# Performance work log

Hardware: AMD Instinct MI355X
Metric: run time of the kernel (lower is better)

The kernel has to match this reference:

```python
import jax, jax.numpy as jnp
import numpy as np

B, N, D, LAT, EC = 1024, 256, 64, 128, 32


def setup_inputs() -> dict:
    key = jax.random.key(0)
    ks = jax.random.split(key, 8)
    s = lambda d: 1.0 / np.sqrt(d)
    return {
        "local_data": jax.random.normal(ks[0], (B, D), jnp.float32),
        "neighbor_data": jax.random.normal(ks[1], (B, N, D), jnp.float32),
        "Wc": jax.random.normal(ks[2], (D, EC), jnp.float32) * s(D),
        "bc": jnp.zeros((EC,), jnp.float32),
        "Wf": jax.random.normal(ks[3], (D, LAT), jnp.float32) * s(D),
        "bf": jnp.zeros((LAT,), jnp.float32),
        "Wa": jax.random.normal(ks[4], (3 * EC, LAT), jnp.float32) * s(3 * EC),
        "ba": jnp.zeros((LAT,), jnp.float32),
        "Wl": jax.random.normal(ks[5], (LAT, LAT), jnp.float32) * s(LAT),
        "bl": jnp.zeros((LAT,), jnp.float32),
    }


def reference(local_data, neighbor_data, Wc, bc, Wf, bf, Wa, ba, Wl, bl):
    # per-neighbor feature encoder: [B,N,LAT]
    enc_feature = jax.nn.relu(jnp.einsum("bnd,dk->bnk", neighbor_data, Wf) + bf)
    # per-neighbor communication encoder: [B,N,EC]
    enc_comm = jax.nn.relu(jnp.einsum("bnd,dk->bnk", neighbor_data, Wc) + bc)
    # self communication embedding: [B,EC]
    enc_comm_self = jax.nn.relu(local_data @ Wc + bc)
    # broadcast self and neighbor-mean to [B,N,EC]
    self_rep = jnp.broadcast_to(enc_comm_self[:, None, :], enc_comm.shape)
    mean_rep = jnp.broadcast_to(enc_comm.mean(axis=1, keepdims=True), enc_comm.shape)
    cat = jnp.concatenate([self_rep, enc_comm, mean_rep], axis=-1)  # [B,N,3*EC]
    # attention: linear then softmax over neighbor axis (dim=-2)
    att = jax.nn.softmax(jnp.einsum("bnc,ck->bnk", cat, Wa) + ba, axis=1)  # [B,N,LAT]
    # attention-weighted sum over neighbors: [B,LAT]
    aggregated = jnp.einsum("bnk,bnk->bk", att, enc_feature)
    # later layer
    return jax.nn.relu(aggregated @ Wl + bl)
```

## Files before the change

### kernel.cpp

```cpp
#include <hip/hip_runtime.h>

#define NB    256
#define DIN   64
#define LATD  128
#define ECD   32

typedef __attribute__((ext_vector_type(8))) __bf16 bf16x8;
typedef __attribute__((ext_vector_type(2))) __bf16 bf16x2;
typedef __attribute__((ext_vector_type(4))) float f32x4;

#define XS_STRIDE 72
#define EC_STRIDE 40
#define WA_STRIDE 40

#define WS_WC  0
#define WS_WF  (32 * 72)
#define WS_WA  (32 * 72 + 128 * 72)
#define WS_WLT_BYTES 33280

#define LOG2E 1.44269504f

#define MFMA(a, b, c) __builtin_amdgcn_mfma_f32_16x16x32_bf16((a), (b), (c), 0, 0, 0)

__device__ __forceinline__ unsigned short f2bf(float f) {
    unsigned u = __builtin_bit_cast(unsigned, f);
    u += 0x7fffu + ((u >> 16) & 1u);
    return (unsigned short)(u >> 16);
}

__device__ __forceinline__ bf16x2 cvt2(float a, float b) {
#if defined(__has_builtin) && __has_builtin(__builtin_amdgcn_cvt_pk_bf16_f32)
    return __builtin_amdgcn_cvt_pk_bf16_f32(a, b);
#else
    union { unsigned short u[2]; bf16x2 v; } r;
    r.u[0] = f2bf(a); r.u[1] = f2bf(b);
    return r.v;
#endif
}

__device__ __forceinline__ bf16x8 pack8(float4 a, float4 b) {
    union { bf16x2 h[4]; bf16x8 v; } r;
    r.h[0] = cvt2(a.x, a.y); r.h[1] = cvt2(a.z, a.w);
    r.h[2] = cvt2(b.x, b.y); r.h[3] = cvt2(b.z, b.w);
    return r.v;
}

__global__ __launch_bounds__(256) void prep_kernel(
    const float* __restrict__ Wc, const float* __restrict__ Wf,
    const float* __restrict__ Wa, const float* __restrict__ Wl,
    unsigned short* __restrict__ ws)
{
    int t = blockIdx.x * blockDim.x + threadIdx.x;
    int stride = gridDim.x * blockDim.x;
    for (int i = t; i < 32 * 64; i += stride) {
        int n = i >> 6, k = i & 63;
        ws[WS_WC + n * XS_STRIDE + k] = f2bf(Wc[k * ECD + n]);
    }
    for (int i = t; i < 128 * 64; i += stride) {
        int n = i >> 6, k = i & 63;
        ws[WS_WF + n * XS_STRIDE + k] = f2bf(Wf[k * LATD + n]);
    }
    for (int i = t; i < 128 * 32; i += stride) {
        int n = i >> 5, k = i & 31;
        ws[WS_WA + n * WA_STRIDE + k] = f2bf(Wa[(ECD + k) * LATD + n] * LOG2E);
    }
    float* wlt = reinterpret_cast<float*>(reinterpret_cast<char*>(ws) + WS_WLT_BYTES);
    for (int i = t; i < 128 * 128; i += stride) {
        int c = i >> 7, k = i & 127;
        wlt[c * 128 + k] = Wl[k * LATD + c];
    }
}

__global__ __launch_bounds__(512, 8) void arm_main(
    const float* __restrict__ xg,
    const float* __restrict__ bcv,
    const float* __restrict__ bfv,
    const float* __restrict__ blv,
    const unsigned short* __restrict__ ws,
    float* __restrict__ out)
{
    __shared__ unsigned short ecs[NB * EC_STRIDE];
    __shared__ float aggnum[8][LATD];
    __shared__ float aggden[8][LATD];
    __shared__ float aggfull[LATD];
    __shared__ float wlpart[4][LATD];

    const int b    = blockIdx.x;
    const int tid  = threadIdx.x;
    const int lane = tid & 63;
    const int w    = tid >> 6;
    const int l15  = lane & 15;
    const int q    = lane >> 4;

    const float* xb = xg + (size_t)b * NB * DIN;
    bf16x8 xfrag[2][2];
    #pragma unroll
    for (int t = 0; t < 2; ++t) {
        const float* p = xb + (w * 32 + t * 16 + l15) * DIN + q * 8;
        float4 a0 = *reinterpret_cast<const float4*>(p);
        float4 a1 = *reinterpret_cast<const float4*>(p + 4);
        float4 a2 = *reinterpret_cast<const float4*>(p + 32);
        float4 a3 = *reinterpret_cast<const float4*>(p + 36);
        xfrag[t][0] = pack8(a0, a1);
        xfrag[t][1] = pack8(a2, a3);
    }

    {
        bf16x8 wfrag[2][2];
        #pragma unroll
        for (int ks = 0; ks < 2; ++ks)
            #pragma unroll
            for (int nb = 0; nb < 2; ++nb)
                wfrag[ks][nb] = *reinterpret_cast<const bf16x8*>(
                    &ws[WS_WC + (nb * 16 + l15) * XS_STRIDE + ks * 32 + q * 8]);

        float bc0 = bcv[l15], bc1 = bcv[16 + l15];
        #pragma unroll
        for (int t = 0; t < 2; ++t) {
            int rowA = w * 32 + t * 16;
            f32x4 a0 = {0.f, 0.f, 0.f, 0.f}, a1 = {0.f, 0.f, 0.f, 0.f};
            #pragma unroll
            for (int ks = 0; ks < 2; ++ks) {
                a0 = MFMA(xfrag[t][ks], wfrag[ks][0], a0);
                a1 = MFMA(xfrag[t][ks], wfrag[ks][1], a1);
            }
            #pragma unroll
            for (int r = 0; r < 4; ++r) {
                int row = rowA + q * 4 + r;
                union { bf16x2 v; unsigned short u[2]; } pr;
                pr.v = cvt2(fmaxf(a0[r] + bc0, 0.f), fmaxf(a1[r] + bc1, 0.f));
                ecs[row * EC_STRIDE + l15]      = pr.u[0];
                ecs[row * EC_STRIDE + 16 + l15] = pr.u[1];
            }
        }
    }

    bf16x8 ecfrag[2];
    #pragma unroll
    for (int t = 0; t < 2; ++t)
        ecfrag[t] = *reinterpret_cast<const bf16x8*>(
            &ecs[(w * 32 + t * 16 + l15) * EC_STRIDE + q * 8]);

    #pragma unroll
    for (int g = 0; g < 8; ++g) {
        bf16x8 wf0 = *reinterpret_cast<const bf16x8*>(
            &ws[WS_WF + (g * 16 + l15) * XS_STRIDE + q * 8]);
        bf16x8 wf1 = *reinterpret_cast<const bf16x8*>(
            &ws[WS_WF + (g * 16 + l15) * XS_STRIDE + 32 + q * 8]);
        bf16x8 wag = *reinterpret_cast<const bf16x8*>(
            &ws[WS_WA + (g * 16 + l15) * WA_STRIDE + q * 8]);

        f32x4 ef[2], lg[2];
        #pragma unroll
        for (int t = 0; t < 2; ++t) {
            f32x4 z = {0.f, 0.f, 0.f, 0.f};
            z = MFMA(xfrag[t][0], wf0, z);
            ef[t] = MFMA(xfrag[t][1], wf1, z);
            f32x4 z2 = {0.f, 0.f, 0.f, 0.f};
            lg[t] = MFMA(ecfrag[t], wag, z2);
        }
        float bfl = bfv[g * 16 + l15];
        float num = 0.f, den = 0.f;
        #pragma unroll
        for (int t = 0; t < 2; ++t)
            #pragma unroll
            for (int r = 0; r < 4; ++r) {
                float e = fmaxf(ef[t][r] + bfl, 0.f);
                float p = exp2f(lg[t][r]);
                num += p * e;
                den += p;
            }
        num += __shfl_xor(num, 16, 64); num += __shfl_xor(num, 32, 64);
        den += __shfl_xor(den, 16, 64); den += __shfl_xor(den, 32, 64);
        if (lane < 16) {
            aggnum[w][g * 16 + lane] = num;
            aggden[w][g * 16 + lane] = den;
        }
    }
    __syncthreads();

    if (tid < 128) {
        float num = 0.f, den = 0.f;
        #pragma unroll
        for (int i = 0; i < 8; ++i) { num += aggnum[i][tid]; den += aggden[i][tid]; }
        aggfull[tid] = num / den;
    }
    __syncthreads();

    {
        const float* wlt = reinterpret_cast<const float*>(
            reinterpret_cast<const char*>(ws) + WS_WLT_BYTES);
        int c = tid & 127, h = tid >> 7;
        const float* wr = wlt + c * 128 + h * 32;
        float acc = 0.f;
        #pragma unroll
        for (int j = 0; j < 8; ++j) {
            float4 v = *reinterpret_cast<const float4*>(wr + j * 4);
            int k = h * 32 + j * 4;
            acc += aggfull[k] * v.x + aggfull[k + 1] * v.y +
                   aggfull[k + 2] * v.z + aggfull[k + 3] * v.w;
        }
        wlpart[h][c] = acc;
    }
    __syncthreads();
    if (tid < 128)
        out[(size_t)b * LATD + tid] =
            fmaxf(wlpart[0][tid] + wlpart[1][tid] + wlpart[2][tid] + wlpart[3][tid]
                  + blv[tid], 0.f);
}

extern "C" void kernel_launch(void* const* d_in, const int* in_sizes, int n_in,
                              void* d_out, int out_size, void* d_ws, size_t ws_size,
                              hipStream_t stream)
{
    const float* xg  = (const float*)d_in[1];
    const float* wc  = (const float*)d_in[2];
    const float* bc_ = (const float*)d_in[3];
    const float* wf  = (const float*)d_in[4];
    const float* bf_ = (const float*)d_in[5];
    const float* wa  = (const float*)d_in[6];
    const float* wl  = (const float*)d_in[8];
    const float* bl_ = (const float*)d_in[9];
    unsigned short* wsp = (unsigned short*)d_ws;
    float* out = (float*)d_out;

    prep_kernel<<<16, 256, 0, stream>>>(wc, wf, wa, wl, wsp);
    arm_main<<<1024, 512, 0, stream>>>(xg, bc_, bf_, bl_, wsp, out);
}
```

Measured before the change: 134.0 us.

## Process two batch rows per block with upfront loads of both inputs

Each block now handles two batch elements and loads both neighbor tiles into registers before computing either, so the second tile's global loads overlap the first element's compute. Wc fragments and the bc/bf biases are hoisted and shared across both elements. The biases are folded into the MFMA accumulator initialisation, and the g loop is no longer force-unrolled. The grid is halved and the launch bound is lowered to 4 blocks, which costs register pressure and parallelism in exchange for the overlap.

```diff
diff --git a/kernel.cpp b/kernel.cpp
--- a/kernel.cpp
+++ b/kernel.cpp
@@ -71,67 +71,38 @@
     }
 }
 
-__global__ __launch_bounds__(512, 8) void arm_main(
-    const float* __restrict__ xg,
-    const float* __restrict__ bcv,
-    const float* __restrict__ bfv,
-    const float* __restrict__ blv,
-    const unsigned short* __restrict__ ws,
-    float* __restrict__ out)
-{
-    __shared__ unsigned short ecs[NB * EC_STRIDE];
-    __shared__ float aggnum[8][LATD];
-    __shared__ float aggden[8][LATD];
-    __shared__ float aggfull[LATD];
-    __shared__ float wlpart[4][LATD];
-
-    const int b    = blockIdx.x;
-    const int tid  = threadIdx.x;
-    const int lane = tid & 63;
-    const int w    = tid >> 6;
-    const int l15  = lane & 15;
-    const int q    = lane >> 4;
-
-    const float* xb = xg + (size_t)b * NB * DIN;
-    bf16x8 xfrag[2][2];
+struct SmemT {
+    unsigned short ecs[NB * EC_STRIDE];
+    float aggnum[8][LATD];
+    float aggden[8][LATD];
+    float aggfull[LATD];
+    float wlpart[4][LATD];
+};
+
+__device__ __forceinline__ void process_b(
+    int b, int w, int lane, int l15, int q, int tid,
+    const bf16x8 xfrag[2][2], const bf16x8 wcfrag[2][2],
+    float bc0, float bc1, const float bfl8[8],
+    const unsigned short* __restrict__ ws, const float* __restrict__ blv,
+    float* __restrict__ out, SmemT& sm)
+{
     #pragma unroll
     for (int t = 0; t < 2; ++t) {
-        const float* p = xb + (w * 32 + t * 16 + l15) * DIN + q * 8;
-        float4 a0 = *reinterpret_cast<const float4*>(p);
-        float4 a1 = *reinterpret_cast<const float4*>(p + 4);
-        float4 a2 = *reinterpret_cast<const float4*>(p + 32);
-        float4 a3 = *reinterpret_cast<const float4*>(p + 36);
-        xfrag[t][0] = pack8(a0, a1);
-        xfrag[t][1] = pack8(a2, a3);
-    }
-
-    {
-        bf16x8 wfrag[2][2];
-        #pragma unroll
-        for (int ks = 0; ks < 2; ++ks)
-            #pragma unroll
-            for (int nb = 0; nb < 2; ++nb)
-                wfrag[ks][nb] = *reinterpret_cast<const bf16x8*>(
-                    &ws[WS_WC + (nb * 16 + l15) * XS_STRIDE + ks * 32 + q * 8]);
-
-        float bc0 = bcv[l15], bc1 = bcv[16 + l15];
-        #pragma unroll
-        for (int t = 0; t < 2; ++t) {
-            int rowA = w * 32 + t * 16;
-            f32x4 a0 = {0.f, 0.f, 0.f, 0.f}, a1 = {0.f, 0.f, 0.f, 0.f};
-            #pragma unroll
-            for (int ks = 0; ks < 2; ++ks) {
-                a0 = MFMA(xfrag[t][ks], wfrag[ks][0], a0);
-                a1 = MFMA(xfrag[t][ks], wfrag[ks][1], a1);
-            }
-            #pragma unroll
-            for (int r = 0; r < 4; ++r) {
-                int row = rowA + q * 4 + r;
-                union { bf16x2 v; unsigned short u[2]; } pr;
-                pr.v = cvt2(fmaxf(a0[r] + bc0, 0.f), fmaxf(a1[r] + bc1, 0.f));
-                ecs[row * EC_STRIDE + l15]      = pr.u[0];
-                ecs[row * EC_STRIDE + 16 + l15] = pr.u[1];
-            }
+        f32x4 a0 = {bc0, bc0, bc0, bc0};
+        f32x4 a1 = {bc1, bc1, bc1, bc1};
+        #pragma unroll
+        for (int ks = 0; ks < 2; ++ks) {
+            a0 = MFMA(xfrag[t][ks], wcfrag[ks][0], a0);
+            a1 = MFMA(xfrag[t][ks], wcfrag[ks][1], a1);
+        }
+        int rowA = w * 32 + t * 16;
+        #pragma unroll
+        for (int r = 0; r < 4; ++r) {
+            int row = rowA + q * 4 + r;
+            union { bf16x2 v; unsigned short u[2]; } pr;
+            pr.v = cvt2(fmaxf(a0[r], 0.f), fmaxf(a1[r], 0.f));
+            sm.ecs[row * EC_STRIDE + l15]      = pr.u[0];
+            sm.ecs[row * EC_STRIDE + 16 + l15] = pr.u[1];
         }
     }
 
@@ -139,9 +110,8 @@
     #pragma unroll
     for (int t = 0; t < 2; ++t)
         ecfrag[t] = *reinterpret_cast<const bf16x8*>(
-            &ecs[(w * 32 + t * 16 + l15) * EC_STRIDE + q * 8]);
-
-    #pragma unroll
+            &sm.ecs[(w * 32 + t * 16 + l15) * EC_STRIDE + q * 8]);
+
     for (int g = 0; g < 8; ++g) {
         bf16x8 wf0 = *reinterpret_cast<const bf16x8*>(
             &ws[WS_WF + (g * 16 + l15) * XS_STRIDE + q * 8]);
@@ -149,32 +119,29 @@
             &ws[WS_WF + (g * 16 + l15) * XS_STRIDE + 32 + q * 8]);
         bf16x8 wag = *reinterpret_cast<const bf16x8*>(
             &ws[WS_WA + (g * 16 + l15) * WA_STRIDE + q * 8]);
-
-        f32x4 ef[2], lg[2];
+        float bfl = bfl8[g];
+
+        float num = 0.f, den = 0.f;
         #pragma unroll
         for (int t = 0; t < 2; ++t) {
-            f32x4 z = {0.f, 0.f, 0.f, 0.f};
+            f32x4 z = {bfl, bfl, bfl, bfl};
             z = MFMA(xfrag[t][0], wf0, z);
-            ef[t] = MFMA(xfrag[t][1], wf1, z);
+            f32x4 ef = MFMA(xfrag[t][1], wf1, z);
             f32x4 z2 = {0.f, 0.f, 0.f, 0.f};
-            lg[t] = MFMA(ecfrag[t], wag, z2);
-        }
-        float bfl = bfv[g * 16 + l15];
-        float num = 0.f, den = 0.f;
-        #pragma unroll
-        for (int t = 0; t < 2; ++t)
+            f32x4 lg = MFMA(ecfrag[t], wag, z2);
             #pragma unroll
             for (int r = 0; r < 4; ++r) {
-                float e = fmaxf(ef[t][r] + bfl, 0.f);
-                float p = exp2f(lg[t][r]);
+                float e = fmaxf(ef[r], 0.f);
+                float p = exp2f(lg[r]);
                 num += p * e;
                 den += p;
             }
+        }
         num += __shfl_xor(num, 16, 64); num += __shfl_xor(num, 32, 64);
         den += __shfl_xor(den, 16, 64); den += __shfl_xor(den, 32, 64);
         if (lane < 16) {
-            aggnum[w][g * 16 + lane] = num;
-            aggden[w][g * 16 + lane] = den;
+            sm.aggnum[w][g * 16 + lane] = num;
+            sm.aggden[w][g * 16 + lane] = den;
         }
     }
     __syncthreads();
@@ -182,8 +149,8 @@
     if (tid < 128) {
         float num = 0.f, den = 0.f;
         #pragma unroll
-        for (int i = 0; i < 8; ++i) { num += aggnum[i][tid]; den += aggden[i][tid]; }
-        aggfull[tid] = num / den;
+        for (int i = 0; i < 8; ++i) { num += sm.aggnum[i][tid]; den += sm.aggden[i][tid]; }
+        sm.aggfull[tid] = num / den;
     }
     __syncthreads();
 
@@ -197,16 +164,89 @@
         for (int j = 0; j < 8; ++j) {
             float4 v = *reinterpret_cast<const float4*>(wr + j * 4);
             int k = h * 32 + j * 4;
-            acc += aggfull[k] * v.x + aggfull[k + 1] * v.y +
-                   aggfull[k + 2] * v.z + aggfull[k + 3] * v.w;
-        }
-        wlpart[h][c] = acc;
+            acc += sm.aggfull[k] * v.x + sm.aggfull[k + 1] * v.y +
+                   sm.aggfull[k + 2] * v.z + sm.aggfull[k + 3] * v.w;
+        }
+        sm.wlpart[h][c] = acc;
     }
     __syncthreads();
     if (tid < 128)
         out[(size_t)b * LATD + tid] =
-            fmaxf(wlpart[0][tid] + wlpart[1][tid] + wlpart[2][tid] + wlpart[3][tid]
-                  + blv[tid], 0.f);
+            fmaxf(sm.wlpart[0][tid] + sm.wlpart[1][tid] + sm.wlpart[2][tid] +
+                  sm.wlpart[3][tid] + blv[tid], 0.f);
+}
+
+__global__ __launch_bounds__(512, 4) void arm_main(
+    const float* __restrict__ xg,
+    const float* __restrict__ bcv,
+    const float* __restrict__ bfv,
+    const float* __restrict__ blv,
+    const unsigned short* __restrict__ ws,
+    float* __restrict__ out)
+{
+    __shared__ SmemT sm;
+
+    const int tid  = threadIdx.x;
+    const int lane = tid & 63;
+    const int w    = tid >> 6;
+    const int l15  = lane & 15;
+    const int q    = lane >> 4;
+    const int b0   = blockIdx.x * 2;
+
+    const float* xb0 = xg + (size_t)b0 * NB * DIN;
+    const float* xb1 = xb0 + NB * DIN;
+
+    float4 r0[2][4];
+    #pragma unroll
+    for (int t = 0; t < 2; ++t) {
+        const float* p = xb0 + (w * 32 + t * 16 + l15) * DIN + q * 8;
+        r0[t][0] = *reinterpret_cast<const float4*>(p);
+        r0[t][1] = *reinterpret_cast<const float4*>(p + 4);
+        r0[t][2] = *reinterpret_cast<const float4*>(p + 32);
+        r0[t][3] = *reinterpret_cast<const float4*>(p + 36);
+    }
+    float4 r1[2][4];
+    #pragma unroll
+    for (int t = 0; t < 2; ++t) {
+        const float* p = xb1 + (w * 32 + t * 16 + l15) * DIN + q * 8;
+        r1[t][0] = *reinterpret_cast<const float4*>(p);
+        r1[t][1] = *reinterpret_cast<const float4*>(p + 4);
+        r1[t][2] = *reinterpret_cast<const float4*>(p + 32);
+        r1[t][3] = *reinterpret_cast<const float4*>(p + 36);
+    }
+
+    bf16x8 wcfrag[2][2];
+    #pragma unroll
+    for (int ks = 0; ks < 2; ++ks)
+        #pragma unroll
+        for (int nb = 0; nb < 2; ++nb)
+            wcfrag[ks][nb] = *reinterpret_cast<const bf16x8*>(
+                &ws[WS_WC + (nb * 16 + l15) * XS_STRIDE + ks * 32 + q * 8]);
+    float bc0 = bcv[l15], bc1 = bcv[16 + l15];
+    float bfl8[8];
+    #pragma unroll
+    for (int g = 0; g < 8; ++g) bfl8[g] = bfv[g * 16 + l15];
+
+    {
+        bf16x8 xfrag[2][2];
+        #pragma unroll
+        for (int t = 0; t < 2; ++t) {
+            xfrag[t][0] = pack8(r0[t][0], r0[t][1]);
+            xfrag[t][1] = pack8(r0[t][2], r0[t][3]);
+        }
+        process_b(b0, w, lane, l15, q, tid, xfrag, wcfrag, bc0, bc1, bfl8,
+                  ws, blv, out, sm);
+    }
+    {
+        bf16x8 xfrag[2][2];
+        #pragma unroll
+        for (int t = 0; t < 2; ++t) {
+            xfrag[t][0] = pack8(r1[t][0], r1[t][1]);
+            xfrag[t][1] = pack8(r1[t][2], r1[t][3]);
+        }
+        process_b(b0 + 1, w, lane, l15, q, tid, xfrag, wcfrag, bc0, bc1, bfl8,
+                  ws, blv, out, sm);
+    }
 }
 
 extern "C" void kernel_launch(void* const* d_in, const int* in_sizes, int n_in,
@@ -225,5 +265,5 @@
     float* out = (float*)d_out;
 
     prep_kernel<<<16, 256, 0, stream>>>(wc, wf, wa, wl, wsp);
-    arm_main<<<1024, 512, 0, stream>>>(xg, bc_, bf_, bl_, wsp, out);
-}
+    arm_main<<<512, 512, 0, stream>>>(xg, bc_, bf_, bl_, wsp, out);
+}
```

Result: slower. 161.1 us (+20.3%).

## Split per-batch work into neighbor chunks with atomic reduction and separate finish kernel

Applied to the files above, without the earlier changes.

Each batch's 256 neighbors are now split across four 256-thread blocks, giving 4096 smaller blocks. Each block produces partial softmax numerator and denominator sums, which are accumulated into a zeroed workspace buffer with atomics. A separate finish kernel then divides numerator by denominator and applies the final Wl projection with ReLU. This is meant to improve occupancy and load balance over the single large 512-thread block per batch, at the cost of an extra memset, atomics, an additional kernel launch and a global round trip for the partial sums. Biases are also folded into the MFMA accumulator initialization.

```diff
diff --git a/kernel.cpp b/kernel.cpp
--- a/kernel.cpp
+++ b/kernel.cpp
@@ -16,7 +16,9 @@
 #define WS_WC  0
 #define WS_WF  (32 * 72)
 #define WS_WA  (32 * 72 + 128 * 72)
-#define WS_WLT_BYTES 33280
+#define WS_WLT_BYTES   33280
+#define WS_ND_BYTES    (33280 + 65536)
+#define WS_TOTAL_BYTES (WS_ND_BYTES + 1024 * 256 * 4)
 
 #define LOG2E 1.44269504f
 
@@ -71,77 +73,62 @@
     }
 }
 
-__global__ __launch_bounds__(512, 8) void arm_main(
+__global__ __launch_bounds__(256, 4) void encode_kernel(
     const float* __restrict__ xg,
     const float* __restrict__ bcv,
     const float* __restrict__ bfv,
-    const float* __restrict__ blv,
     const unsigned short* __restrict__ ws,
-    float* __restrict__ out)
-{
-    __shared__ unsigned short ecs[NB * EC_STRIDE];
-    __shared__ float aggnum[8][LATD];
-    __shared__ float aggden[8][LATD];
-    __shared__ float aggfull[LATD];
-    __shared__ float wlpart[4][LATD];
-
-    const int b    = blockIdx.x;
+    float* __restrict__ numden)
+{
+    __shared__ unsigned short ecs[4 * 16 * EC_STRIDE];
+    __shared__ float aggnum[4][LATD];
+    __shared__ float aggden[4][LATD];
+
+    const int blk  = blockIdx.x;
+    const int b    = blk >> 2;
+    const int chnk = blk & 3;
     const int tid  = threadIdx.x;
     const int lane = tid & 63;
     const int w    = tid >> 6;
     const int l15  = lane & 15;
     const int q    = lane >> 4;
 
-    const float* xb = xg + (size_t)b * NB * DIN;
-    bf16x8 xfrag[2][2];
-    #pragma unroll
-    for (int t = 0; t < 2; ++t) {
-        const float* p = xb + (w * 32 + t * 16 + l15) * DIN + q * 8;
-        float4 a0 = *reinterpret_cast<const float4*>(p);
-        float4 a1 = *reinterpret_cast<const float4*>(p + 4);
-        float4 a2 = *reinterpret_cast<const float4*>(p + 32);
-        float4 a3 = *reinterpret_cast<const float4*>(p + 36);
-        xfrag[t][0] = pack8(a0, a1);
-        xfrag[t][1] = pack8(a2, a3);
-    }
+    const float* p = xg + ((size_t)b * NB + chnk * 64 + w * 16 + l15) * DIN + q * 8;
+    float4 a0 = *reinterpret_cast<const float4*>(p);
+    float4 a1 = *reinterpret_cast<const float4*>(p + 4);
+    float4 a2 = *reinterpret_cast<const float4*>(p + 32);
+    float4 a3 = *reinterpret_cast<const float4*>(p + 36);
+    bf16x8 xf0 = pack8(a0, a1);
+    bf16x8 xf1 = pack8(a2, a3);
 
     {
-        bf16x8 wfrag[2][2];
+        float bc0 = bcv[l15], bc1 = bcv[16 + l15];
+        f32x4 e0 = {bc0, bc0, bc0, bc0};
+        f32x4 e1 = {bc1, bc1, bc1, bc1};
         #pragma unroll
-        for (int ks = 0; ks < 2; ++ks)
-            #pragma unroll
-            for (int nb = 0; nb < 2; ++nb)
-                wfrag[ks][nb] = *reinterpret_cast<const bf16x8*>(
-                    &ws[WS_WC + (nb * 16 + l15) * XS_STRIDE + ks * 32 + q * 8]);
-
-        float bc0 = bcv[l15], bc1 = bcv[16 + l15];
+        for (int ks = 0; ks < 2; ++ks) {
+            bf16x8 wc0 = *reinterpret_cast<const bf16x8*>(
+                &ws[WS_WC + l15 * XS_STRIDE + ks * 32 + q * 8]);
+            bf16x8 wc1 = *reinterpret_cast<const bf16x8*>(
+                &ws[WS_WC + (16 + l15) * XS_STRIDE + ks * 32 + q * 8]);
+            bf16x8 xa = ks ? xf1 : xf0;
+            e0 = MFMA(xa, wc0, e0);
+            e1 = MFMA(xa, wc1, e1);
+        }
+        unsigned short* ecw = &ecs[w * 16 * EC_STRIDE];
         #pragma unroll
-        for (int t = 0; t < 2; ++t) {
-            int rowA = w * 32 + t * 16;
-            f32x4 a0 = {0.f, 0.f, 0.f, 0.f}, a1 = {0.f, 0.f, 0.f, 0.f};
-            #pragma unroll
-            for (int ks = 0; ks < 2; ++ks) {
-                a0 = MFMA(xfrag[t][ks], wfrag[ks][0], a0);
-                a1 = MFMA(xfrag[t][ks], wfrag[ks][1], a1);
-            }
-            #pragma unroll
-            for (int r = 0; r < 4; ++r) {
-                int row = rowA + q * 4 + r;
-                union { bf16x2 v; unsigned short u[2]; } pr;
-                pr.v = cvt2(fmaxf(a0[r] + bc0, 0.f), fmaxf(a1[r] + bc1, 0.f));
-                ecs[row * EC_STRIDE + l15]      = pr.u[0];
-                ecs[row * EC_STRIDE + 16 + l15] = pr.u[1];
-            }
-        }
-    }
-
-    bf16x8 ecfrag[2];
-    #pragma unroll
-    for (int t = 0; t < 2; ++t)
-        ecfrag[t] = *reinterpret_cast<const bf16x8*>(
-            &ecs[(w * 32 + t * 16 + l15) * EC_STRIDE + q * 8]);
-
-    #pragma unroll
+        for (int r = 0; r < 4; ++r) {
+            int row = q * 4 + r;
+            union { bf16x2 v; unsigned short u[2]; } pr;
+            pr.v = cvt2(fmaxf(e0[r], 0.f), fmaxf(e1[r], 0.f));
+            ecw[row * EC_STRIDE + l15]      = pr.u[0];
+            ecw[row * EC_STRIDE + 16 + l15] = pr.u[1];
+        }
+    }
+
+    bf16x8 ecfrag = *reinterpret_cast<const bf16x8*>(
+        &ecs[(w * 16 + l15) * EC_STRIDE + q * 8]);
+
     for (int g = 0; g < 8; ++g) {
         bf16x8 wf0 = *reinterpret_cast<const bf16x8*>(
             &ws[WS_WF + (g * 16 + l15) * XS_STRIDE + q * 8]);
@@ -149,27 +136,22 @@
             &ws[WS_WF + (g * 16 + l15) * XS_STRIDE + 32 + q * 8]);
         bf16x8 wag = *reinterpret_cast<const bf16x8*>(
             &ws[WS_WA + (g * 16 + l15) * WA_STRIDE + q * 8]);
-
-        f32x4 ef[2], lg[2];
-        #pragma unroll
-        for (int t = 0; t < 2; ++t) {
-            f32x4 z = {0.f, 0.f, 0.f, 0.f};
-            z = MFMA(xfrag[t][0], wf0, z);
-            ef[t] = MFMA(xfrag[t][1], wf1, z);
-            f32x4 z2 = {0.f, 0.f, 0.f, 0.f};
-            lg[t] = MFMA(ecfrag[t], wag, z2);
-        }
         float bfl = bfv[g * 16 + l15];
+
+        f32x4 z = {bfl, bfl, bfl, bfl};
+        z = MFMA(xf0, wf0, z);
+        f32x4 ef = MFMA(xf1, wf1, z);
+        f32x4 zz = {0.f, 0.f, 0.f, 0.f};
+        f32x4 lg = MFMA(ecfrag, wag, zz);
+
         float num = 0.f, den = 0.f;
         #pragma unroll
-        for (int t = 0; t < 2; ++t)
-            #pragma unroll
-            for (int r = 0; r < 4; ++r) {
-                float e = fmaxf(ef[t][r] + bfl, 0.f);
-                float p = exp2f(lg[t][r]);
-                num += p * e;
-                den += p;
-            }
+        for (int r = 0; r < 4; ++r) {
+            float e = fmaxf(ef[r], 0.f);
+            float pe = exp2f(lg[r]);
+            num += pe * e;
+            den += pe;
+        }
         num += __shfl_xor(num, 16, 64); num += __shfl_xor(num, 32, 64);
         den += __shfl_xor(den, 16, 64); den += __shfl_xor(den, 32, 64);
         if (lane < 16) {
@@ -180,33 +162,45 @@
     __syncthreads();
 
     if (tid < 128) {
-        float num = 0.f, den = 0.f;
-        #pragma unroll
-        for (int i = 0; i < 8; ++i) { num += aggnum[i][tid]; den += aggden[i][tid]; }
-        aggfull[tid] = num / den;
+        float v = aggnum[0][tid] + aggnum[1][tid] + aggnum[2][tid] + aggnum[3][tid];
+        atomicAdd(&numden[(size_t)b * 256 + tid], v);
+    } else {
+        int k = tid - 128;
+        float v = aggden[0][k] + aggden[1][k] + aggden[2][k] + aggden[3][k];
+        atomicAdd(&numden[(size_t)b * 256 + 128 + k], v);
+    }
+}
+
+__global__ __launch_bounds__(256) void finish_kernel(
+    const float* __restrict__ numden,
+    const unsigned short* __restrict__ ws,
+    const float* __restrict__ blv,
+    float* __restrict__ out)
+{
+    __shared__ float agg_s[2][LATD];
+    const int tid = threadIdx.x;
+    const int b0  = blockIdx.x * 2;
+
+    {
+        int lb = tid >> 7, k = tid & 127;
+        const float* nd = numden + (size_t)(b0 + lb) * 256;
+        agg_s[lb][k] = nd[k] / nd[128 + k];
     }
     __syncthreads();
 
-    {
-        const float* wlt = reinterpret_cast<const float*>(
-            reinterpret_cast<const char*>(ws) + WS_WLT_BYTES);
-        int c = tid & 127, h = tid >> 7;
-        const float* wr = wlt + c * 128 + h * 32;
-        float acc = 0.f;
-        #pragma unroll
-        for (int j = 0; j < 8; ++j) {
-            float4 v = *reinterpret_cast<const float4*>(wr + j * 4);
-            int k = h * 32 + j * 4;
-            acc += aggfull[k] * v.x + aggfull[k + 1] * v.y +
-                   aggfull[k + 2] * v.z + aggfull[k + 3] * v.w;
-        }
-        wlpart[h][c] = acc;
-    }
-    __syncthreads();
-    if (tid < 128)
-        out[(size_t)b * LATD + tid] =
-            fmaxf(wlpart[0][tid] + wlpart[1][tid] + wlpart[2][tid] + wlpart[3][tid]
-                  + blv[tid], 0.f);
+    const float* wlt = reinterpret_cast<const float*>(
+        reinterpret_cast<const char*>(ws) + WS_WLT_BYTES);
+    int lb = tid >> 7, c = tid & 127;
+    const float* wr = wlt + c * 128;
+    float acc = blv[c];
+    #pragma unroll
+    for (int j = 0; j < 32; ++j) {
+        float4 v = *reinterpret_cast<const float4*>(wr + j * 4);
+        int k = j * 4;
+        acc += agg_s[lb][k] * v.x + agg_s[lb][k + 1] * v.y +
+               agg_s[lb][k + 2] * v.z + agg_s[lb][k + 3] * v.w;
+    }
+    out[(size_t)(b0 + lb) * LATD + c] = fmaxf(acc, 0.f);
 }
 
 extern "C" void kernel_launch(void* const* d_in, const int* in_sizes, int n_in,
@@ -222,8 +216,11 @@
     const float* wl  = (const float*)d_in[8];
     const float* bl_ = (const float*)d_in[9];
     unsigned short* wsp = (unsigned short*)d_ws;
+    float* numden = reinterpret_cast<float*>(reinterpret_cast<char*>(d_ws) + WS_ND_BYTES);
     float* out = (float*)d_out;
 
+    hipMemsetAsync(numden, 0, 1024 * 256 * sizeof(float), stream);
     prep_kernel<<<16, 256, 0, stream>>>(wc, wf, wa, wl, wsp);
-    arm_main<<<1024, 512, 0, stream>>>(xg, bc_, bf_, bl_, wsp, out);
-}
+    encode_kernel<<<4096, 256, 0, stream>>>(xg, bc_, bf_, wsp, numden);
+    finish_kernel<<<512, 256, 0, stream>>>(numden, wsp, bl_, out);
+}
```

After: 142.7 us. +6.5%, slower.
